# Performance work log

Hardware: AMD Instinct MI355X
Metric: run time of the kernel (lower is better)

Reference implementation:

```python
import jax, jax.numpy as jnp
import numpy as np

N = 1_000_000          # query points
L = 6                  # positional encoding terms
ND = 3                 # n_dims
C = 16                 # n_features
G = 96                 # feature grid resolution per axis
NODES = 128            # decoder width
IN_DIM = C + L * ND * 2  # 52
VOL_MIN, VOL_MAX = 0.0, 1.0


def setup_inputs() -> dict:
    key = jax.random.key(0)
    ks = jax.random.split(key, 8)
    x = jax.random.uniform(ks[0], (N, ND), jnp.float32, minval=-1.0, maxval=1.0)
    feature_grid = jax.random.uniform(ks[1], (C, G, G, G), jnp.float32)  # torch.rand init
    s = 0.05
    w_in = jax.random.normal(ks[2], (IN_DIM, NODES), jnp.float32) * s
    w_h0 = jax.random.normal(ks[3], (NODES, NODES), jnp.float32) * s
    w_h1 = jax.random.normal(ks[4], (NODES, NODES), jnp.float32) * s
    w_h2 = jax.random.normal(ks[5], (NODES, NODES), jnp.float32) * s
    w_out = jax.random.normal(ks[6], (NODES, 1), jnp.float32) * s
    return {"x": x, "feature_grid": feature_grid, "w_in": w_in,
            "w_h0": w_h0, "w_h1": w_h1, "w_h2": w_h2, "w_out": w_out}


def _trilinear(grid, pts):
    """grid_sample 3D, bilinear, align_corners=True. grid [C,D,H,W], pts [N,3]
    with channel order (x->W, y->H, z->D) as in torch. Returns [N, C]."""
    Cc, D, H, W = grid.shape
    fx = (pts[:, 0] + 1.0) * 0.5 * (W - 1)
    fy = (pts[:, 1] + 1.0) * 0.5 * (H - 1)
    fz = (pts[:, 2] + 1.0) * 0.5 * (D - 1)
    x0 = jnp.floor(fx); y0 = jnp.floor(fy); z0 = jnp.floor(fz)
    tx = fx - x0; ty = fy - y0; tz = fz - z0
    x0i = jnp.clip(x0.astype(jnp.int32), 0, W - 1); x1i = jnp.clip(x0i + 1, 0, W - 1)
    y0i = jnp.clip(y0.astype(jnp.int32), 0, H - 1); y1i = jnp.clip(y0i + 1, 0, H - 1)
    z0i = jnp.clip(z0.astype(jnp.int32), 0, D - 1); z1i = jnp.clip(z0i + 1, 0, D - 1)

    def g(zi, yi, xi):
        return grid[:, zi, yi, xi].T  # [N, C]

    c000 = g(z0i, y0i, x0i); c001 = g(z0i, y0i, x1i)
    c010 = g(z0i, y1i, x0i); c011 = g(z0i, y1i, x1i)
    c100 = g(z1i, y0i, x0i); c101 = g(z1i, y0i, x1i)
    c110 = g(z1i, y1i, x0i); c111 = g(z1i, y1i, x1i)
    tx = tx[:, None]; ty = ty[:, None]; tz = tz[:, None]
    c00 = c000 * (1 - tx) + c001 * tx
    c01 = c010 * (1 - tx) + c011 * tx
    c10 = c100 * (1 - tx) + c101 * tx
    c11 = c110 * (1 - tx) + c111 * tx
    c0 = c00 * (1 - ty) + c01 * ty
    c1 = c10 * (1 - ty) + c11 * ty
    return c0 * (1 - tz) + c1 * tz


def _pos_enc(pts):
    # [N, L*ND*2]: sin/cos of pi * 2^k * x for k in 0..L-1
    freqs = (jnp.pi * (2.0 ** jnp.arange(L, dtype=jnp.float32)))  # [L]
    ang = pts[:, None, :] * freqs[None, :, None]                   # [N, L, ND]
    pe = jnp.concatenate([jnp.sin(ang), jnp.cos(ang)], axis=-1)    # [N, L, 2*ND]
    return pe.reshape(pts.shape[0], -1)


def reference(x, feature_grid, w_in, w_h0, w_h1, w_h2, w_out):
    feats = _trilinear(feature_grid, x)          # [N, C]
    pe = _pos_enc(x)                             # [N, 2*L*ND]
    h = jnp.concatenate([pe, feats], axis=1)     # [N, IN_DIM]
    h = jax.nn.relu(h @ w_in)
    h = jax.nn.relu(h @ w_h0)
    h = jax.nn.relu(h @ w_h1)
    h = jax.nn.relu(h @ w_h2)
    y = h @ w_out                                # [N, 1]
    return y * (VOL_MAX - VOL_MIN) + VOL_MIN
```

## Files before the change

### kernel.cpp

```cpp
#include <hip/hip_runtime.h>
#include <stdint.h>

typedef unsigned int uint;
typedef unsigned short ushort;

#define GD   96
#define GD2  (GD*GD)
#define GSP  (GD*GD*GD)
#define NPTS 1000000
#define WIN_ELTS 8192
#define WH_ELTS  16384
#define WFRAG_OFF (GSP*16)
#define WFRAG_N  (WIN_ELTS + 3*WH_ELTS)

#define NSLAB 8
#define SLABZ 12
#define CAP   131072
#define NSLOT (NSLAB*CAP)

#define XS_BYTE   ((size_t)(WFRAG_OFF + WFRAG_N) * 2)
#define OID_BYTE  (XS_BYTE + (size_t)NSLOT * 16)
#define CUR_BYTE  (OID_BYTE + (size_t)NSLOT * 4)

#define PW   128
#define ROWB 272
#define LDS_BYTES (4*PW*ROWB)

typedef __attribute__((ext_vector_type(8))) short short8;
typedef __attribute__((ext_vector_type(4))) float f32x4;

__device__ __forceinline__ uint f2bf(float x) {
  uint u = __float_as_uint(x);
  return (u + 0x7fffu + ((u >> 16) & 1u)) >> 16;
}

__global__ void k_grid_pack(const float* __restrict__ g, ushort* __restrict__ o) {
  int sp = blockIdx.x * 256 + threadIdx.x;
  uint pk[8];
#pragma unroll
  for (int c = 0; c < 16; c += 2) {
    float a = g[(size_t)c * GSP + sp];
    float b = g[(size_t)(c + 1) * GSP + sp];
    pk[c >> 1] = f2bf(a) | (f2bf(b) << 16);
  }
  uint4* dst = (uint4*)(o + (size_t)sp * 16);
  dst[0] = make_uint4(pk[0], pk[1], pk[2], pk[3]);
  dst[1] = make_uint4(pk[4], pk[5], pk[6], pk[7]);
}

__global__ void k_w_pack(const float* __restrict__ win, const float* __restrict__ h0,
                         const float* __restrict__ h1, const float* __restrict__ h2,
                         ushort* __restrict__ o) {
  int tid = blockIdx.x * 256 + threadIdx.x;
  int lane = (tid >> 3) & 63, j = tid & 7;
  int q = lane >> 4, cc = lane & 15;
  float v;
  if (tid < WIN_ELTS) {
    int blk = tid >> 9;
    int t = blk >> 1, s = blk & 1;
    int k = s * 32 + q * 8 + j, n = t * 16 + cc;
    v = (k < 52) ? win[k * 128 + n] : 0.f;
  } else {
    int f2 = tid - WIN_ELTS;
    int l = f2 >> 14, r = f2 & 16383;
    int blk = r >> 9;
    int t = blk >> 2, s = blk & 3;
    int k = s * 32 + q * 8 + j, n = t * 16 + cc;
    const float* w = (l == 0) ? h0 : ((l == 1) ? h1 : h2);
    v = w[k * 128 + n];
  }
  o[tid] = (ushort)f2bf(v);
}

__global__ void k_prefill(const float* __restrict__ x, float4* __restrict__ xs,
                          int* __restrict__ oid, int* __restrict__ cursor) {
  int id = blockIdx.x * 256 + threadIdx.x;
  float lx = x[(NPTS - 1) * 3 + 0];
  float ly = x[(NPTS - 1) * 3 + 1];
  float lz = x[(NPTS - 1) * 3 + 2];
  xs[id] = make_float4(lx, ly, lz, 0.f);
  oid[id] = NPTS - 1;
  if (id < NSLAB) cursor[id] = id * CAP;
}

__global__ void k_scatter(const float* __restrict__ x, float4* __restrict__ xs,
                          int* __restrict__ oid, int* __restrict__ cursor) {
  __shared__ int lc[NSLAB], lb[NSLAB];
  const int tid = threadIdx.x;
  if (tid < NSLAB) lc[tid] = 0;
  __syncthreads();
  const int pbase = blockIdx.x * 4096;
  int rk[16], sl[16];
#pragma unroll
  for (int i = 0; i < 16; ++i) {
    int p = pbase + i * 256 + tid;
    int pc = min(p, NPTS - 1);
    float pz = x[pc * 3 + 2];
    int z0i = min(max((int)floorf((pz + 1.0f) * 0.5f * 95.0f), 0), 95);
    int s = z0i / SLABZ;
    sl[i] = s;
    rk[i] = (p < NPTS) ? atomicAdd(&lc[s], 1) : -1;
  }
  __syncthreads();
  if (tid < NSLAB) lb[tid] = atomicAdd(&cursor[tid], lc[tid]);
  __syncthreads();
#pragma unroll
  for (int i = 0; i < 16; ++i) {
    int p = pbase + i * 256 + tid;
    if (p < NPTS) {
      int slot = lb[sl[i]] + rk[i];
      xs[slot] = make_float4(x[p * 3 + 0], x[p * 3 + 1], x[p * 3 + 2], 0.f);
      oid[slot] = p;
    }
  }
}

#define ACC8(off, U, W) {                                  \
  fv[(off)+0] += (W) * __uint_as_float((U).x << 16);       \
  fv[(off)+1] += (W) * __uint_as_float((U).x & 0xffff0000u);\
  fv[(off)+2] += (W) * __uint_as_float((U).y << 16);       \
  fv[(off)+3] += (W) * __uint_as_float((U).y & 0xffff0000u);\
  fv[(off)+4] += (W) * __uint_as_float((U).z << 16);       \
  fv[(off)+5] += (W) * __uint_as_float((U).z & 0xffff0000u);\
  fv[(off)+6] += (W) * __uint_as_float((U).w << 16);       \
  fv[(off)+7] += (W) * __uint_as_float((U).w & 0xffff0000u);\
}

#define MFMA(A,B,C) __builtin_amdgcn_mfma_f32_16x16x32_bf16((A),(B),(C),0,0,0)

#define HREAD(P, A0,A1,A2,A3, B0,B1,B2,B3) {               \
  const char* ap_ = act + ((P)*32 + c) * ROWB + q * 16;    \
  const char* bp_ = ap_ + 16 * ROWB;                       \
  A0 = *(const short8*)(ap_);       A1 = *(const short8*)(ap_ + 64);  \
  A2 = *(const short8*)(ap_ + 128); A3 = *(const short8*)(ap_ + 192); \
  B0 = *(const short8*)(bp_);       B1 = *(const short8*)(bp_ + 64);  \
  B2 = *(const short8*)(bp_ + 128); B3 = *(const short8*)(bp_ + 192); \
}

#define HZERO2(AVA, AVB) { _Pragma("unroll")               \
  for (int t = 0; t < 8; ++t) { AVA[t] = f32x4{0.f,0.f,0.f,0.f}; AVB[t] = f32x4{0.f,0.f,0.f,0.f}; } }

#define HMFMA2(A0,A1,A2,A3, B0,B1,B2,B3, AVA, AVB) { _Pragma("unroll") \
  for (int t = 0; t < 8; ++t) {                            \
    AVA[t] = MFMA(A0, bw[t*4+0], AVA[t]);                  \
    AVA[t] = MFMA(A1, bw[t*4+1], AVA[t]);                  \
    AVA[t] = MFMA(A2, bw[t*4+2], AVA[t]);                  \
    AVA[t] = MFMA(A3, bw[t*4+3], AVA[t]);                  \
    AVB[t] = MFMA(B0, bw[t*4+0], AVB[t]);                  \
    AVB[t] = MFMA(B1, bw[t*4+1], AVB[t]);                  \
    AVB[t] = MFMA(B2, bw[t*4+2], AVB[t]);                  \
    AVB[t] = MFMA(B3, bw[t*4+3], AVB[t]); } }

#define IMFMA2(A0,A1, B0,B1, AVA, AVB) { _Pragma("unroll") \
  for (int t = 0; t < 8; ++t) {                            \
    AVA[t] = MFMA(A0, bwin[t*2+0], AVA[t]);                \
    AVA[t] = MFMA(A1, bwin[t*2+1], AVA[t]);                \
    AVB[t] = MFMA(B0, bwin[t*2+0], AVB[t]);                \
    AVB[t] = MFMA(B1, bwin[t*2+1], AVB[t]); } }

#define HEPI(P, AVA, AVB) {                                \
  char* yA_ = act + ((P)*32 + q * 4) * ROWB + c * 2;       \
  char* yB_ = yA_ + 16 * ROWB;                             \
  _Pragma("unroll") for (int t = 0; t < 8; ++t)            \
    _Pragma("unroll") for (int r = 0; r < 4; ++r) {        \
      *(ushort*)(yA_ + r * ROWB + t * 32) = (ushort)f2bf(fmaxf(AVA[t][r], 0.f)); \
      *(ushort*)(yB_ + r * ROWB + t * 32) = (ushort)f2bf(fmaxf(AVB[t][r], 0.f)); } }

#define OEPI(P, AVA, AVB) { _Pragma("unroll")              \
  for (int r = 0; r < 4; ++r) {                            \
    float yA = 0.f, yB = 0.f;                              \
    _Pragma("unroll") for (int t = 0; t < 8; ++t) {        \
      yA += fmaxf(AVA[t][r], 0.f) * wo[t];                 \
      yB += fmaxf(AVB[t][r], 0.f) * wo[t]; }               \
    yA += __shfl_xor(yA, 1, 64); yA += __shfl_xor(yA, 2, 64); \
    yA += __shfl_xor(yA, 4, 64); yA += __shfl_xor(yA, 8, 64); \
    yB += __shfl_xor(yB, 1, 64); yB += __shfl_xor(yB, 2, 64); \
    yB += __shfl_xor(yB, 4, 64); yB += __shfl_xor(yB, 8, 64); \
    if (c == r) {                                          \
      int slotA = base + (P)*32 + q * 4 + r;               \
      out[oid[slotA]] = yA;                                \
      out[oid[slotA + 16]] = yB; } } }

__global__ __launch_bounds__(256, 1) void k_main(
    const float4* __restrict__ xs, const int* __restrict__ oid,
    const float* __restrict__ wout,
    const ushort* __restrict__ gridb, const ushort* __restrict__ wfrag,
    float* __restrict__ out) {
  extern __shared__ char smem[];
  const int wave = threadIdx.x >> 6;
  const int lane = threadIdx.x & 63;
  const int q = lane >> 4, c = lane & 15;
  char* act = smem + wave * (PW * ROWB);
  const int b = blockIdx.x;
  const int base = (b & 7) * CAP + (b >> 3) * 512 + wave * PW;

  short8 bwin[16];
#pragma unroll
  for (int f = 0; f < 16; ++f)
    bwin[f] = *(const short8*)(wfrag + f * 512 + lane * 8);
  float wo[8];
#pragma unroll
  for (int t = 0; t < 8; ++t) wo[t] = wout[t * 16 + c];

#pragma unroll
  for (int pp = 0; pp < 2; ++pp) {
    const int p = pp * 64 + lane;
    const float4 c4 = xs[base + p];
    const float px = c4.x;
    const float py = c4.y;
    const float pz = c4.z;
    float fx = (px + 1.0f) * 0.5f * 95.0f;
    float fy = (py + 1.0f) * 0.5f * 95.0f;
    float fz = (pz + 1.0f) * 0.5f * 95.0f;
    float x0f = floorf(fx), y0f = floorf(fy), z0f = floorf(fz);
    float tx = fx - x0f, ty = fy - y0f, tz = fz - z0f;
    int x0i = min(max((int)x0f, 0), 95);
    int y0i = min(max((int)y0f, 0), 95);
    int z0i = min(max((int)z0f, 0), 95);
    int x1i = min(x0i + 1, 95);
    int y1i = min(y0i + 1, 95);
    int z1i = min(z0i + 1, 95);
    float fv[16];
#pragma unroll
    for (int k = 0; k < 16; ++k) fv[k] = 0.f;
#pragma unroll
    for (int dz = 0; dz < 2; ++dz) {
      const int zi = dz ? z1i : z0i;
      const float wz = dz ? tz : (1.f - tz);
#pragma unroll
      for (int dy = 0; dy < 2; ++dy) {
        const int yi = dy ? y1i : y0i;
        const float wzy = wz * (dy ? ty : (1.f - ty));
        const ushort* r0 = gridb + (size_t)(zi * GD2 + yi * GD + x0i) * 16;
        const ushort* r1 = gridb + (size_t)(zi * GD2 + yi * GD + x1i) * 16;
        uint4 a0 = *(const uint4*)r0;
        uint4 a1 = *(const uint4*)(r0 + 8);
        uint4 b0 = *(const uint4*)r1;
        uint4 b1 = *(const uint4*)(r1 + 8);
        const float w0 = wzy * (1.f - tx), w1 = wzy * tx;
        ACC8(0, a0, w0); ACC8(8, a1, w0);
        ACC8(0, b0, w1); ACC8(8, b1, w1);
      }
    }
    float row[64];
#pragma unroll
    for (int i = 0; i < 6; ++i) {
      const float fr = 3.14159265358979323846f * (float)(1 << i);
      row[i*6+0] = __sinf(px*fr); row[i*6+1] = __sinf(py*fr); row[i*6+2] = __sinf(pz*fr);
      row[i*6+3] = __cosf(px*fr); row[i*6+4] = __cosf(py*fr); row[i*6+5] = __cosf(pz*fr);
    }
#pragma unroll
    for (int k = 0; k < 16; ++k) row[36 + k] = fv[k];
#pragma unroll
    for (int k = 52; k < 64; ++k) row[k] = 0.f;
    char* dst = act + p * ROWB;
#pragma unroll
    for (int k = 0; k < 64; k += 8) {
      uint u0 = f2bf(row[k+0]) | (f2bf(row[k+1]) << 16);
      uint u1 = f2bf(row[k+2]) | (f2bf(row[k+3]) << 16);
      uint u2 = f2bf(row[k+4]) | (f2bf(row[k+5]) << 16);
      uint u3 = f2bf(row[k+6]) | (f2bf(row[k+7]) << 16);
      *(uint4*)(dst + k * 2) = make_uint4(u0, u1, u2, u3);
    }
  }
  asm volatile("s_waitcnt lgkmcnt(0)" ::: "memory");

  {
    short8 xA0, xA1, xB0, xB1, yA0, yA1, yB0, yB1;
    f32x4 ac0A[8], ac0B[8], ac1A[8], ac1B[8];
    {
      const char* ap_ = act + c * ROWB + q * 16;
      const char* bp_ = ap_ + 16 * ROWB;
      xA0 = *(const short8*)(ap_); xA1 = *(const short8*)(ap_ + 64);
      xB0 = *(const short8*)(bp_); xB1 = *(const short8*)(bp_ + 64);
    }
    HZERO2(ac0A, ac0B);
    IMFMA2(xA0, xA1, xB0, xB1, ac0A, ac0B);
    {
      const char* ap_ = act + (32 + c) * ROWB + q * 16;
      const char* bp_ = ap_ + 16 * ROWB;
      yA0 = *(const short8*)(ap_); yA1 = *(const short8*)(ap_ + 64);
      yB0 = *(const short8*)(bp_); yB1 = *(const short8*)(bp_ + 64);
    }
    HZERO2(ac1A, ac1B);
    HEPI(0, ac0A, ac0B);
    IMFMA2(yA0, yA1, yB0, yB1, ac1A, ac1B);
    {
      const char* ap_ = act + (64 + c) * ROWB + q * 16;
      const char* bp_ = ap_ + 16 * ROWB;
      xA0 = *(const short8*)(ap_); xA1 = *(const short8*)(ap_ + 64);
      xB0 = *(const short8*)(bp_); xB1 = *(const short8*)(bp_ + 64);
    }
    HZERO2(ac0A, ac0B);
    HEPI(1, ac1A, ac1B);
    IMFMA2(xA0, xA1, xB0, xB1, ac0A, ac0B);
    {
      const char* ap_ = act + (96 + c) * ROWB + q * 16;
      const char* bp_ = ap_ + 16 * ROWB;
      yA0 = *(const short8*)(ap_); yA1 = *(const short8*)(ap_ + 64);
      yB0 = *(const short8*)(bp_); yB1 = *(const short8*)(bp_ + 64);
    }
    HZERO2(ac1A, ac1B);
    HEPI(2, ac0A, ac0B);
    IMFMA2(yA0, yA1, yB0, yB1, ac1A, ac1B);
    HEPI(3, ac1A, ac1B);
  }
  asm volatile("s_waitcnt lgkmcnt(0)" ::: "memory");

  for (int l = 0; l < 3; ++l) {
    const ushort* wl = wfrag + WIN_ELTS + l * WH_ELTS;
    short8 bw[32];
#pragma unroll
    for (int f = 0; f < 32; ++f)
      bw[f] = *(const short8*)(wl + f * 512 + lane * 8);
    short8 xA0, xA1, xA2, xA3, xB0, xB1, xB2, xB3;
    short8 yA0, yA1, yA2, yA3, yB0, yB1, yB2, yB3;
    f32x4 ac0A[8], ac0B[8], ac1A[8], ac1B[8];
    if (l < 2) {
      HREAD(0, xA0, xA1, xA2, xA3, xB0, xB1, xB2, xB3);
      HZERO2(ac0A, ac0B);
      HMFMA2(xA0, xA1, xA2, xA3, xB0, xB1, xB2, xB3, ac0A, ac0B);

      HREAD(1, yA0, yA1, yA2, yA3, yB0, yB1, yB2, yB3);
      HZERO2(ac1A, ac1B);
      HEPI(0, ac0A, ac0B);
      HMFMA2(yA0, yA1, yA2, yA3, yB0, yB1, yB2, yB3, ac1A, ac1B);

      HREAD(2, xA0, xA1, xA2, xA3, xB0, xB1, xB2, xB3);
      HZERO2(ac0A, ac0B);
      HEPI(1, ac1A, ac1B);
      HMFMA2(xA0, xA1, xA2, xA3, xB0, xB1, xB2, xB3, ac0A, ac0B);

      HREAD(3, yA0, yA1, yA2, yA3, yB0, yB1, yB2, yB3);
      HZERO2(ac1A, ac1B);
      HEPI(2, ac0A, ac0B);
      HMFMA2(yA0, yA1, yA2, yA3, yB0, yB1, yB2, yB3, ac1A, ac1B);

      HEPI(3, ac1A, ac1B);
      asm volatile("s_waitcnt lgkmcnt(0)" ::: "memory");
    } else {
      HREAD(0, xA0, xA1, xA2, xA3, xB0, xB1, xB2, xB3);
      HZERO2(ac0A, ac0B);
      HMFMA2(xA0, xA1, xA2, xA3, xB0, xB1, xB2, xB3, ac0A, ac0B);

      HREAD(1, yA0, yA1, yA2, yA3, yB0, yB1, yB2, yB3);
      HZERO2(ac1A, ac1B);
      OEPI(0, ac0A, ac0B);
      HMFMA2(yA0, yA1, yA2, yA3, yB0, yB1, yB2, yB3, ac1A, ac1B);

      HREAD(2, xA0, xA1, xA2, xA3, xB0, xB1, xB2, xB3);
      HZERO2(ac0A, ac0B);
      OEPI(1, ac1A, ac1B);
      HMFMA2(xA0, xA1, xA2, xA3, xB0, xB1, xB2, xB3, ac0A, ac0B);

      HREAD(3, yA0, yA1, yA2, yA3, yB0, yB1, yB2, yB3);
      HZERO2(ac1A, ac1B);
      OEPI(2, ac0A, ac0B);
      HMFMA2(yA0, yA1, yA2, yA3, yB0, yB1, yB2, yB3, ac1A, ac1B);

      OEPI(3, ac1A, ac1B);
    }
  }
}

extern "C" void kernel_launch(void* const* d_in, const int* in_sizes, int n_in,
                              void* d_out, int out_size, void* d_ws, size_t ws_size,
                              hipStream_t stream) {
  const float* x    = (const float*)d_in[0];
  const float* fg   = (const float*)d_in[1];
  const float* win  = (const float*)d_in[2];
  const float* wh0  = (const float*)d_in[3];
  const float* wh1  = (const float*)d_in[4];
  const float* wh2  = (const float*)d_in[5];
  const float* wout = (const float*)d_in[6];
  float* out = (float*)d_out;

  char* wsb = (char*)d_ws;
  ushort* gridb  = (ushort*)d_ws;
  ushort* wfrag  = (ushort*)d_ws + WFRAG_OFF;
  float4* xs     = (float4*)(wsb + XS_BYTE);
  int*    oid    = (int*)(wsb + OID_BYTE);
  int*    cursor = (int*)(wsb + CUR_BYTE);

  k_grid_pack<<<GSP / 256, 256, 0, stream>>>(fg, gridb);
  k_w_pack<<<(WIN_ELTS + 3 * WH_ELTS) / 256, 256, 0, stream>>>(win, wh0, wh1, wh2, wfrag);
  k_prefill<<<NSLOT / 256, 256, 0, stream>>>(x, xs, oid, cursor);
  k_scatter<<<(NPTS + 4095) / 4096, 256, 0, stream>>>(x, xs, oid, cursor);

  k_main<<<NSLAB * (CAP / 512), 256, LDS_BYTES, stream>>>(xs, oid, wout, gridb, wfrag, out);
}
```

Baseline: 386.3 us.

## Drop z-slab point binning and fuse grid/weight packing into one kernel

Removes the prefill and scatter kernels that bucketed points by z-slab, so the main kernel reads x directly in original order and writes outputs without the oid indirection. The two packing kernels are merged into a single launch. This cuts launches, the scatter traffic and atomics, and the padded slots processed by the main kernel. The cost is losing spatial locality for the grid gathers, since random point order may hurt cache hit rates on the bf16 feature grid.

```diff
diff --git a/kernel.cpp b/kernel.cpp
--- a/kernel.cpp
+++ b/kernel.cpp
@@ -11,21 +11,14 @@
 #define WIN_ELTS 8192
 #define WH_ELTS  16384
 #define WFRAG_OFF (GSP*16)
-#define WFRAG_N  (WIN_ELTS + 3*WH_ELTS)
-
-#define NSLAB 8
-#define SLABZ 12
-#define CAP   131072
-#define NSLOT (NSLAB*CAP)
-
-#define XS_BYTE   ((size_t)(WFRAG_OFF + WFRAG_N) * 2)
-#define OID_BYTE  (XS_BYTE + (size_t)NSLOT * 16)
-#define CUR_BYTE  (OID_BYTE + (size_t)NSLOT * 4)
 
 #define PW   128
 #define ROWB 272
 #define LDS_BYTES (4*PW*ROWB)
 
+#define GP_BLOCKS (GSP/256)
+#define WP_BLOCKS ((WIN_ELTS+3*WH_ELTS)/256)
+
 typedef __attribute__((ext_vector_type(8))) short short8;
 typedef __attribute__((ext_vector_type(4))) float f32x4;
 
@@ -34,84 +27,43 @@
   return (u + 0x7fffu + ((u >> 16) & 1u)) >> 16;
 }
 
-__global__ void k_grid_pack(const float* __restrict__ g, ushort* __restrict__ o) {
-  int sp = blockIdx.x * 256 + threadIdx.x;
-  uint pk[8];
-#pragma unroll
-  for (int c = 0; c < 16; c += 2) {
-    float a = g[(size_t)c * GSP + sp];
-    float b = g[(size_t)(c + 1) * GSP + sp];
-    pk[c >> 1] = f2bf(a) | (f2bf(b) << 16);
-  }
-  uint4* dst = (uint4*)(o + (size_t)sp * 16);
-  dst[0] = make_uint4(pk[0], pk[1], pk[2], pk[3]);
-  dst[1] = make_uint4(pk[4], pk[5], pk[6], pk[7]);
-}
-
-__global__ void k_w_pack(const float* __restrict__ win, const float* __restrict__ h0,
-                         const float* __restrict__ h1, const float* __restrict__ h2,
-                         ushort* __restrict__ o) {
-  int tid = blockIdx.x * 256 + threadIdx.x;
-  int lane = (tid >> 3) & 63, j = tid & 7;
-  int q = lane >> 4, cc = lane & 15;
-  float v;
-  if (tid < WIN_ELTS) {
-    int blk = tid >> 9;
-    int t = blk >> 1, s = blk & 1;
-    int k = s * 32 + q * 8 + j, n = t * 16 + cc;
-    v = (k < 52) ? win[k * 128 + n] : 0.f;
+__global__ void k_pre(const float* __restrict__ g,
+                      const float* __restrict__ win, const float* __restrict__ h0,
+                      const float* __restrict__ h1, const float* __restrict__ h2,
+                      ushort* __restrict__ ogrid, ushort* __restrict__ owf) {
+  const int blk = blockIdx.x;
+  if (blk < GP_BLOCKS) {
+    int sp = blk * 256 + threadIdx.x;
+    uint pk[8];
+#pragma unroll
+    for (int c = 0; c < 16; c += 2) {
+      float a = g[(size_t)c * GSP + sp];
+      float b = g[(size_t)(c + 1) * GSP + sp];
+      pk[c >> 1] = f2bf(a) | (f2bf(b) << 16);
+    }
+    uint4* dst = (uint4*)(ogrid + (size_t)sp * 16);
+    dst[0] = make_uint4(pk[0], pk[1], pk[2], pk[3]);
+    dst[1] = make_uint4(pk[4], pk[5], pk[6], pk[7]);
   } else {
-    int f2 = tid - WIN_ELTS;
-    int l = f2 >> 14, r = f2 & 16383;
-    int blk = r >> 9;
-    int t = blk >> 2, s = blk & 3;
-    int k = s * 32 + q * 8 + j, n = t * 16 + cc;
-    const float* w = (l == 0) ? h0 : ((l == 1) ? h1 : h2);
-    v = w[k * 128 + n];
-  }
-  o[tid] = (ushort)f2bf(v);
-}
-
-__global__ void k_prefill(const float* __restrict__ x, float4* __restrict__ xs,
-                          int* __restrict__ oid, int* __restrict__ cursor) {
-  int id = blockIdx.x * 256 + threadIdx.x;
-  float lx = x[(NPTS - 1) * 3 + 0];
-  float ly = x[(NPTS - 1) * 3 + 1];
-  float lz = x[(NPTS - 1) * 3 + 2];
-  xs[id] = make_float4(lx, ly, lz, 0.f);
-  oid[id] = NPTS - 1;
-  if (id < NSLAB) cursor[id] = id * CAP;
-}
-
-__global__ void k_scatter(const float* __restrict__ x, float4* __restrict__ xs,
-                          int* __restrict__ oid, int* __restrict__ cursor) {
-  __shared__ int lc[NSLAB], lb[NSLAB];
-  const int tid = threadIdx.x;
-  if (tid < NSLAB) lc[tid] = 0;
-  __syncthreads();
-  const int pbase = blockIdx.x * 4096;
-  int rk[16], sl[16];
-#pragma unroll
-  for (int i = 0; i < 16; ++i) {
-    int p = pbase + i * 256 + tid;
-    int pc = min(p, NPTS - 1);
-    float pz = x[pc * 3 + 2];
-    int z0i = min(max((int)floorf((pz + 1.0f) * 0.5f * 95.0f), 0), 95);
-    int s = z0i / SLABZ;
-    sl[i] = s;
-    rk[i] = (p < NPTS) ? atomicAdd(&lc[s], 1) : -1;
-  }
-  __syncthreads();
-  if (tid < NSLAB) lb[tid] = atomicAdd(&cursor[tid], lc[tid]);
-  __syncthreads();
-#pragma unroll
-  for (int i = 0; i < 16; ++i) {
-    int p = pbase + i * 256 + tid;
-    if (p < NPTS) {
-      int slot = lb[sl[i]] + rk[i];
-      xs[slot] = make_float4(x[p * 3 + 0], x[p * 3 + 1], x[p * 3 + 2], 0.f);
-      oid[slot] = p;
-    }
+    int tid = (blk - GP_BLOCKS) * 256 + threadIdx.x;
+    int lane = (tid >> 3) & 63, j = tid & 7;
+    int q = lane >> 4, cc = lane & 15;
+    float v;
+    if (tid < WIN_ELTS) {
+      int b2 = tid >> 9;
+      int t = b2 >> 1, s = b2 & 1;
+      int k = s * 32 + q * 8 + j, n = t * 16 + cc;
+      v = (k < 52) ? win[k * 128 + n] : 0.f;
+    } else {
+      int f2 = tid - WIN_ELTS;
+      int l = f2 >> 14, r = f2 & 16383;
+      int b2 = r >> 9;
+      int t = b2 >> 2, s = b2 & 3;
+      int k = s * 32 + q * 8 + j, n = t * 16 + cc;
+      const float* w = (l == 0) ? h0 : ((l == 1) ? h1 : h2);
+      v = w[k * 128 + n];
+    }
+    owf[tid] = (ushort)f2bf(v);
   }
 }
 
@@ -177,13 +129,13 @@
     yB += __shfl_xor(yB, 1, 64); yB += __shfl_xor(yB, 2, 64); \
     yB += __shfl_xor(yB, 4, 64); yB += __shfl_xor(yB, 8, 64); \
     if (c == r) {                                          \
-      int slotA = base + (P)*32 + q * 4 + r;               \
-      out[oid[slotA]] = yA;                                \
-      out[oid[slotA + 16]] = yB; } } }
+      int gpo = base + (P)*32 + q * 4 + r;                 \
+      if (gpo < NPTS) out[gpo] = yA;                       \
+      int gpo2 = gpo + 16;                                 \
+      if (gpo2 < NPTS) out[gpo2] = yB; } } }
 
 __global__ __launch_bounds__(256, 1) void k_main(
-    const float4* __restrict__ xs, const int* __restrict__ oid,
-    const float* __restrict__ wout,
+    const float* __restrict__ x, const float* __restrict__ wout,
     const ushort* __restrict__ gridb, const ushort* __restrict__ wfrag,
     float* __restrict__ out) {
   extern __shared__ char smem[];
@@ -191,8 +143,7 @@
   const int lane = threadIdx.x & 63;
   const int q = lane >> 4, c = lane & 15;
   char* act = smem + wave * (PW * ROWB);
-  const int b = blockIdx.x;
-  const int base = (b & 7) * CAP + (b >> 3) * 512 + wave * PW;
+  const int base = blockIdx.x * (4 * PW) + wave * PW;
 
   short8 bwin[16];
 #pragma unroll
@@ -205,10 +156,11 @@
 #pragma unroll
   for (int pp = 0; pp < 2; ++pp) {
     const int p = pp * 64 + lane;
-    const float4 c4 = xs[base + p];
-    const float px = c4.x;
-    const float py = c4.y;
-    const float pz = c4.z;
+    const int gp = base + p;
+    const int gpc = min(gp, NPTS - 1);
+    const float px = x[gpc * 3 + 0];
+    const float py = x[gpc * 3 + 1];
+    const float pz = x[gpc * 3 + 2];
     float fx = (px + 1.0f) * 0.5f * 95.0f;
     float fy = (py + 1.0f) * 0.5f * 95.0f;
     float fz = (pz + 1.0f) * 0.5f * 95.0f;
@@ -375,17 +327,11 @@
   const float* wout = (const float*)d_in[6];
   float* out = (float*)d_out;
 
-  char* wsb = (char*)d_ws;
-  ushort* gridb  = (ushort*)d_ws;
-  ushort* wfrag  = (ushort*)d_ws + WFRAG_OFF;
-  float4* xs     = (float4*)(wsb + XS_BYTE);
-  int*    oid    = (int*)(wsb + OID_BYTE);
-  int*    cursor = (int*)(wsb + CUR_BYTE);
-
-  k_grid_pack<<<GSP / 256, 256, 0, stream>>>(fg, gridb);
-  k_w_pack<<<(WIN_ELTS + 3 * WH_ELTS) / 256, 256, 0, stream>>>(win, wh0, wh1, wh2, wfrag);
-  k_prefill<<<NSLOT / 256, 256, 0, stream>>>(x, xs, oid, cursor);
-  k_scatter<<<(NPTS + 4095) / 4096, 256, 0, stream>>>(x, xs, oid, cursor);
-
-  k_main<<<NSLAB * (CAP / 512), 256, LDS_BYTES, stream>>>(xs, oid, wout, gridb, wfrag, out);
-}
+  ushort* gridb = (ushort*)d_ws;
+  ushort* wfrag = (ushort*)d_ws + WFRAG_OFF;
+
+  k_pre<<<GP_BLOCKS + WP_BLOCKS, 256, 0, stream>>>(fg, win, wh0, wh1, wh2, gridb, wfrag);
+
+  const int nblk = (NPTS + 4 * PW - 1) / (4 * PW);
+  k_main<<<nblk, 256, LDS_BYTES, stream>>>(x, wout, gridb, wfrag, out);
+}
```

Result: faster. 375.1 us, median of 2 (-2.9%).
